# Optimization experiments

Measured on AMD Instinct MI355X. Metric: run time of the kernel, lower is better.

Reference implementation:

```python
import jax, jax.numpy as jnp
import numpy as np


def setup_inputs() -> dict:
    key = jax.random.key(0)
    k0, k1 = jax.random.split(key)
    B, S, T = 32, 512, 128
    return {
        "crf_score_0": jax.random.normal(k0, (B, S + 1, T, T), dtype=jnp.float32),
        "crf_score_1": jax.random.normal(k1, (B, S + 1, T), dtype=jnp.float32),
        "sof": 126,
        "eof": 127,
    }


def reference(crf_score_0, crf_score_1, sof, eof):
    # crf_score_0: [B, S+1, T, T], crf_score_1: [B, S+1, T]
    # Initial scores (note: original multiplies, not adds, at step 0)
    forscores = crf_score_0[:, 0, sof, :] * crf_score_1[:, 0, :]  # [B, T]

    # Move seq axis first for scan: [S, B, T, T] and [S, B, T]
    c0 = jnp.moveaxis(crf_score_0[:, 1:], 0, 1)
    c1 = jnp.moveaxis(crf_score_1[:, 1:], 0, 1)

    def fwd_step(fs, xs):
        t0, t1 = xs  # [B, T, T], [B, T]
        # cur[b, i, j] = fs[b, i] + t1[b, j] + t0[b, i, j]
        cur = fs[:, :, None] + t1[:, None, :] + t0
        new_fs = jnp.max(cur, axis=1)            # [B, T]
        bp = jnp.argmax(cur, axis=1).astype(jnp.int32)  # [B, T]
        return new_fs, bp

    _, back_points = jax.lax.scan(fwd_step, forscores, (c0, c1))  # bps: [S, B, T]

    # Backtrack exactly as the original loop: pointer starts at bp[-1][:, eof],
    # then for idx = S-1 .. 0: pointer = bp[idx][b, pointer]; decode[:, idx] = pointer.
    ptr0 = back_points[-1][:, eof]  # [B]

    def bwd_step(ptr, bp_t):
        new = jnp.take_along_axis(bp_t, ptr[:, None], axis=1)[:, 0]
        return new, new

    _, dec = jax.lax.scan(bwd_step, ptr0, back_points, reverse=True)  # [S, B]
    return dec.T.astype(jnp.int32)  # [B, S] decoded label indices
```

## Files before the change

### kernel.cpp

```cpp
#include <hip/hip_runtime.h>


constexpr int S   = 512;
constexpr int T   = 128;
constexpr int NSL = 8;
constexpr int CW  = 16;

using u64 = unsigned long long;
using u32 = unsigned int;

__device__ __forceinline__ void bar_lds() {
    asm volatile("s_waitcnt lgkmcnt(0)" ::: "memory");
    __builtin_amdgcn_s_barrier();
}
__device__ __forceinline__ u32 flipf(u32 u)   { return u ^ (0x80000000u | (u32)((int)u >> 31)); }
__device__ __forceinline__ u32 unflipf(u32 y) { return y ^ (0x80000000u | ~(u32)((int)y >> 31)); }
__device__ __forceinline__ u64 aload(const u64* p) {
    return __hip_atomic_load(p, __ATOMIC_RELAXED, __HIP_MEMORY_SCOPE_AGENT);
}
__device__ __forceinline__ void astore(u64* p, u64 v) {
    __hip_atomic_store(p, v, __ATOMIC_RELAXED, __HIP_MEMORY_SCOPE_AGENT);
}

#define GLDS(srcp, dstp) \
    __builtin_amdgcn_global_load_lds( \
        (const __attribute__((address_space(1))) void*)(srcp), \
        (__attribute__((address_space(3))) void*)(dstp), 16, 0, 0)

__global__ __launch_bounds__(256, 1)
void viterbi_fwdj(const float* __restrict__ c0, const float* __restrict__ c1,
                  const int* __restrict__ sofp,
                  u64* __restrict__ pub,
                  unsigned char* __restrict__ bp)
{
    __shared__ float fs_lds[T];
    __shared__ float t0s[2][T * CW];
    __shared__ u64   wpart[2][CW];

    const int g    = blockIdx.x;
    const int b    = g & 31;
    const int k    = g >> 5;
    const int tid  = (int)threadIdx.x;
    const int lane = tid & 63;

    const float* c0b = c0 + (size_t)b * (S + 1) * T * T;
    const float* c1b = c1 + (size_t)b * (S + 1) * T;
    u64* pubB = pub + (size_t)b * 2 * T;

    const bool is_cmp = tid >= 128;
    const int  ct  = tid - 128;
    const int  j   = ct & 15;
    const int  rb  = ct >> 4;
    const int  wv2 = (tid >> 6) - 2;

    auto STAGE = [&](int ss, int buf) {
        const float* srcbase = c0b + (size_t)ss * T * T + (size_t)k * CW;
        #pragma unroll
        for (int it = 0; it < 4; ++it) {
            const int q   = wv2 * 4 + it;
            const int row = q * 16 + (lane >> 2);
            const float* src = srcbase + (size_t)row * T + (lane & 3) * 4;
            float* dst = &t0s[buf][q * 256];
            GLDS(src, dst);
        }
    };

    if (tid < T) fs_lds[tid] = c0b[(size_t)sofp[0] * T + tid] * c1b[tid];
    float t1c = 0.f, t1n = 0.f;
    if (is_cmp) {
        STAGE(1, 1);
        t1c = c1b[(size_t)1 * T + k * CW + j];
    }
    asm volatile("s_waitcnt vmcnt(0)" ::: "memory");
    bar_lds();

    for (int s = 1; s <= S; ++s) {
        const int par = s & 1;

        if (is_cmp) {
            const float* tp = &t0s[par][0];
            const int r0 = rb * 16;
            u64 key;
            {
                float v = (fs_lds[r0] + t1c) + tp[r0 * CW + j];
                key = ((u64)flipf(__float_as_uint(v)) << 32) | (u32)(255 - r0);
            }
            #pragma unroll
            for (int r = 1; r < 16; ++r) {
                const int row = r0 + r;
                float v = (fs_lds[row] + t1c) + tp[row * CW + j];
                u64 kk = ((u64)flipf(__float_as_uint(v)) << 32) | (u32)(255 - row);
                if (kk > key) key = kk;
            }
            { u64 p = __shfl_xor(key, 16, 64); if (p > key) key = p; }
            { u64 p = __shfl_xor(key, 32, 64); if (p > key) key = p; }
            if ((ct & 63) < 16) wpart[wv2][j] = key;

            if (s < S) {
                STAGE(s + 1, par ^ 1);
                t1n = c1b[(size_t)(s + 1) * T + k * CW + j];
            }
        }
        bar_lds();

        if (is_cmp && ct < 16) {
            u64 kk = wpart[0][j];
            u64 k1 = wpart[1][j];
            if (k1 > kk) kk = k1;
            const u32 vb = unflipf((u32)(kk >> 32));
            const int ii = 255 - (int)(kk & 0xFFu);
            astore(&pubB[(size_t)par * T + k * CW + j], ((u64)vb << 32) | (u32)s);
            bp[((size_t)b * S + (s - 1)) * T + k * CW + j] = (unsigned char)ii;
            fs_lds[k * CW + j] = __uint_as_float(vb);
        }
        if (!is_cmp && (tid >> 4) != k) {
            const u64* p = &pubB[(size_t)par * T + tid];
            u64 v;
            do { v = aload(p); } while ((u32)v != (u32)s);
            fs_lds[tid] = __uint_as_float((u32)(v >> 32));
        }
        if (is_cmp) asm volatile("s_waitcnt vmcnt(0)" ::: "memory");
        bar_lds();

        t1c = t1n;
    }
}

__global__ __launch_bounds__(1024, 1)
void viterbi_bwd(const unsigned char* __restrict__ bp,
                 const int* __restrict__ eofp, int* __restrict__ out)
{
    __shared__ unsigned char lbp[S][T];
    const int b   = blockIdx.x;
    const int tid = (int)threadIdx.x;

    const uint4* s4 = (const uint4*)(bp + (size_t)b * S * T);
    uint4* d4 = (uint4*)&lbp[0][0];
    #pragma unroll
    for (int it = 0; it < 4; ++it) d4[tid + it * 1024] = s4[tid + it * 1024];
    __syncthreads();

    if (tid == 0) {
        int ptr = lbp[S - 1][eofp[0]];
        for (int idx = S - 1; idx >= 0; --idx) {
            ptr = lbp[idx][ptr];
            out[(size_t)b * S + idx] = ptr;
        }
    }
}

__global__ __launch_bounds__(1024, 1)
void viterbi_fused_fb(const float* __restrict__ c0, const float* __restrict__ c1,
                      const int* __restrict__ sofp, const int* __restrict__ eofp,
                      int* __restrict__ out)
{
    __shared__ float fs[2][T];
    __shared__ float pmax[32][T];
    __shared__ int   parg[32][T];
    __shared__ unsigned char bpl[S][T];

    const int b   = blockIdx.x;
    const int tid = (int)threadIdx.x;
    const int jq  = tid & 31;
    const int gg2 = tid >> 5;
    const int col = jq * 4;
    const int row = gg2 * 4;

    const float* c0b = c0 + (size_t)b * (S + 1) * T * T;
    const float* c1b = c1 + (size_t)b * (S + 1) * T;

    if (tid < T) {
        const int sof = sofp[0];
        fs[0][tid] = c0b[(size_t)sof * T + tid] * c1b[tid];
    }
    __syncthreads();

    const float* t0p = c0b + (size_t)T * T;
    float4 a0 = *(const float4*)(t0p + (size_t)(row + 0) * T + col);
    float4 a1 = *(const float4*)(t0p + (size_t)(row + 1) * T + col);
    float4 a2 = *(const float4*)(t0p + (size_t)(row + 2) * T + col);
    float4 a3 = *(const float4*)(t0p + (size_t)(row + 3) * T + col);
    float4 tv = *(const float4*)(c1b + T + col);

    int p = 0;
    for (int s = 1; s <= S; ++s) {
        float4 b0 = make_float4(0.f,0.f,0.f,0.f), b1 = b0, b2 = b0, b3 = b0, bt = b0;
        if (s < S) {
            const float* n0 = c0b + (size_t)(s + 1) * T * T;
            b0 = *(const float4*)(n0 + (size_t)(row + 0) * T + col);
            b1 = *(const float4*)(n0 + (size_t)(row + 1) * T + col);
            b2 = *(const float4*)(n0 + (size_t)(row + 2) * T + col);
            b3 = *(const float4*)(n0 + (size_t)(row + 3) * T + col);
            bt = *(const float4*)(c1b + (size_t)(s + 1) * T + col);
        }
        const float f0 = fs[p][row + 0];
        const float f1 = fs[p][row + 1];
        const float f2 = fs[p][row + 2];
        const float f3 = fs[p][row + 3];

        float bx, by, bz, bw; int ix, iy, iz, iw; float v;
        bx = (f0 + tv.x) + a0.x; ix = row;
        by = (f0 + tv.y) + a0.y; iy = row;
        bz = (f0 + tv.z) + a0.z; iz = row;
        bw = (f0 + tv.w) + a0.w; iw = row;
        v = (f1 + tv.x) + a1.x; if (v > bx) { bx = v; ix = row + 1; }
        v = (f1 + tv.y) + a1.y; if (v > by) { by = v; iy = row + 1; }
        v = (f1 + tv.z) + a1.z; if (v > bz) { bz = v; iz = row + 1; }
        v = (f1 + tv.w) + a1.w; if (v > bw) { bw = v; iw = row + 1; }
        v = (f2 + tv.x) + a2.x; if (v > bx) { bx = v; ix = row + 2; }
        v = (f2 + tv.y) + a2.y; if (v > by) { by = v; iy = row + 2; }
        v = (f2 + tv.z) + a2.z; if (v > bz) { bz = v; iz = row + 2; }
        v = (f2 + tv.w) + a2.w; if (v > bw) { bw = v; iw = row + 2; }
        v = (f3 + tv.x) + a3.x; if (v > bx) { bx = v; ix = row + 3; }
        v = (f3 + tv.y) + a3.y; if (v > by) { by = v; iy = row + 3; }
        v = (f3 + tv.z) + a3.z; if (v > bz) { bz = v; iz = row + 3; }
        v = (f3 + tv.w) + a3.w; if (v > bw) { bw = v; iw = row + 3; }

        *(float4*)&pmax[gg2][col] = make_float4(bx, by, bz, bw);
        *(int4*)  &parg[gg2][col] = make_int4(ix, iy, iz, iw);
        __syncthreads();

        if (tid < T) {
            float bb = pmax[0][tid];
            int   ii = parg[0][tid];
            #pragma unroll
            for (int qq2 = 1; qq2 < 32; ++qq2) {
                float vv = pmax[qq2][tid];
                if (vv > bb) { bb = vv; ii = parg[qq2][tid]; }
            }
            fs[p ^ 1][tid] = bb;
            bpl[s - 1][tid] = (unsigned char)ii;
        }
        __syncthreads();
        p ^= 1;
        a0 = b0; a1 = b1; a2 = b2; a3 = b3; tv = bt;
    }

    if (tid == 0) {
        const int eof = eofp[0];
        int ptr = bpl[S - 1][eof];
        for (int idx = S - 1; idx >= 0; --idx) {
            ptr = bpl[idx][ptr];
            out[(size_t)b * S + idx] = ptr;
        }
    }
}

extern "C" void kernel_launch(void* const* d_in, const int* in_sizes, int n_in,
                              void* d_out, int out_size, void* d_ws, size_t ws_size,
                              hipStream_t stream)
{
    const float* c0  = (const float*)d_in[0];
    const float* c1  = (const float*)d_in[1];
    const int*   sof = (const int*)d_in[2];
    const int*   eof = (const int*)d_in[3];
    int*         out = (int*)d_out;

    const int B = in_sizes[1] / ((S + 1) * T);

    const size_t pub_b = (size_t)B * 2 * T * 8;
    const size_t bp_b  = (size_t)B * S * T;
    if (B == 32 && ws_size >= pub_b + bp_b) {
        u64* pubw = (u64*)d_ws;
        unsigned char* bpw = (unsigned char*)d_ws + pub_b;
        viterbi_fwdj<<<dim3(B * NSL), dim3(256), 0, stream>>>(c0, c1, sof, pubw, bpw);
        viterbi_bwd<<<dim3(B), dim3(1024), 0, stream>>>(bpw, eof, out);
    } else {
        viterbi_fused_fb<<<dim3(B), dim3(1024), 0, stream>>>(c0, c1, sof, eof, out);
    }
}
```

Before: 846.9 us.

## Split forward Viterbi into dedicated poller and register-prefetching compute warps

The forward kernel is reorganised so the first 128 threads only poll remote slices' published scores into a double-buffered LDS array, while compute threads each own one column and 16 rows. Those compute threads hold two steps of transition data in registers instead of staging tiles through LDS with async global-to-LDS loads. The row reduction now uses in-register argmax plus three shuffles, which removes the wpart LDS reduction and one barrier per step. Publication switches to an atomic exchange. The trade-off is strided scalar global loads (16 per thread per step) and heavier register use, in exchange for a shorter per-step critical path.

```diff
diff --git a/kernel.cpp b/kernel.cpp
--- a/kernel.cpp
+++ b/kernel.cpp
@@ -4,7 +4,6 @@
 constexpr int S   = 512;
 constexpr int T   = 128;
 constexpr int NSL = 8;
-constexpr int CW  = 16;
 
 using u64 = unsigned long long;
 using u32 = unsigned int;
@@ -18,111 +17,112 @@
 __device__ __forceinline__ u64 aload(const u64* p) {
     return __hip_atomic_load(p, __ATOMIC_RELAXED, __HIP_MEMORY_SCOPE_AGENT);
 }
-__device__ __forceinline__ void astore(u64* p, u64 v) {
-    __hip_atomic_store(p, v, __ATOMIC_RELAXED, __HIP_MEMORY_SCOPE_AGENT);
-}
-
-#define GLDS(srcp, dstp) \
-    __builtin_amdgcn_global_load_lds( \
-        (const __attribute__((address_space(1))) void*)(srcp), \
-        (__attribute__((address_space(3))) void*)(dstp), 16, 0, 0)
+__device__ __forceinline__ void apub(u64* p, u64 v) {
+    (void)__hip_atomic_exchange(p, v, __ATOMIC_RELAXED, __HIP_MEMORY_SCOPE_AGENT);
+}
 
 __global__ __launch_bounds__(256, 1)
-void viterbi_fwdj(const float* __restrict__ c0, const float* __restrict__ c1,
+void viterbi_fwdx(const float* __restrict__ c0, const float* __restrict__ c1,
                   const int* __restrict__ sofp,
                   u64* __restrict__ pub,
                   unsigned char* __restrict__ bp)
 {
-    __shared__ float fs_lds[T];
-    __shared__ float t0s[2][T * CW];
-    __shared__ u64   wpart[2][CW];
-
-    const int g    = blockIdx.x;
-    const int b    = g & 31;
-    const int k    = g >> 5;
-    const int tid  = (int)threadIdx.x;
-    const int lane = tid & 63;
+    __shared__ float fs[2][T];
+
+    const int g   = blockIdx.x;
+    const int b   = g & 31;
+    const int k   = g >> 5;
+    const int tid = (int)threadIdx.x;
 
     const float* c0b = c0 + (size_t)b * (S + 1) * T * T;
     const float* c1b = c1 + (size_t)b * (S + 1) * T;
     u64* pubB = pub + (size_t)b * 2 * T;
 
-    const bool is_cmp = tid >= 128;
-    const int  ct  = tid - 128;
-    const int  j   = ct & 15;
-    const int  rb  = ct >> 4;
-    const int  wv2 = (tid >> 6) - 2;
-
-    auto STAGE = [&](int ss, int buf) {
-        const float* srcbase = c0b + (size_t)ss * T * T + (size_t)k * CW;
+    if (tid < 128) {
+        const int  col    = tid;
+        const bool remote = (col >> 4) != k;
+        fs[0][col] = c0b[(size_t)sofp[0] * T + col] * c1b[col];
+        bar_lds();
+        for (int s = 1; s <= S; ++s) {
+            if (remote) {
+                const u64* p = &pubB[(size_t)(s & 1) * T + col];
+                u64 v;
+                do { v = aload(p); } while ((u32)v != (u32)s);
+                fs[s & 1][col] = __uint_as_float((u32)(v >> 32));
+            }
+            bar_lds();
+        }
+    } else {
+        const int ct  = tid - 128;
+        const int jj  = ct >> 3;
+        const int ih  = ct & 7;
+        const int col = k * 16 + jj;
+        const int r0  = 16 * ih;
+        const u32 tieb = (u32)(255 - r0);
+
+        const float* pA = c0b + (size_t)1 * T * T + (size_t)r0 * T + col;
+        const float* pB = pA + T * T;
+        float a[16], c[16];
         #pragma unroll
-        for (int it = 0; it < 4; ++it) {
-            const int q   = wv2 * 4 + it;
-            const int row = q * 16 + (lane >> 2);
-            const float* src = srcbase + (size_t)row * T + (lane & 3) * 4;
-            float* dst = &t0s[buf][q * 256];
-            GLDS(src, dst);
-        }
-    };
-
-    if (tid < T) fs_lds[tid] = c0b[(size_t)sofp[0] * T + tid] * c1b[tid];
-    float t1c = 0.f, t1n = 0.f;
-    if (is_cmp) {
-        STAGE(1, 1);
-        t1c = c1b[(size_t)1 * T + k * CW + j];
-    }
-    asm volatile("s_waitcnt vmcnt(0)" ::: "memory");
-    bar_lds();
-
-    for (int s = 1; s <= S; ++s) {
-        const int par = s & 1;
-
-        if (is_cmp) {
-            const float* tp = &t0s[par][0];
-            const int r0 = rb * 16;
-            u64 key;
-            {
-                float v = (fs_lds[r0] + t1c) + tp[r0 * CW + j];
-                key = ((u64)flipf(__float_as_uint(v)) << 32) | (u32)(255 - r0);
-            }
-            #pragma unroll
-            for (int r = 1; r < 16; ++r) {
-                const int row = r0 + r;
-                float v = (fs_lds[row] + t1c) + tp[row * CW + j];
-                u64 kk = ((u64)flipf(__float_as_uint(v)) << 32) | (u32)(255 - row);
-                if (kk > key) key = kk;
-            }
-            { u64 p = __shfl_xor(key, 16, 64); if (p > key) key = p; }
-            { u64 p = __shfl_xor(key, 32, 64); if (p > key) key = p; }
-            if ((ct & 63) < 16) wpart[wv2][j] = key;
-
-            if (s < S) {
-                STAGE(s + 1, par ^ 1);
-                t1n = c1b[(size_t)(s + 1) * T + k * CW + j];
-            }
-        }
+        for (int i = 0; i < 16; ++i) a[i] = pA[i * T];
+        #pragma unroll
+        for (int i = 0; i < 16; ++i) c[i] = pB[i * T];
+        float tA = c1b[(size_t)1 * T + col];
+        float tB = c1b[(size_t)2 * T + col];
+        unsigned char* bpc = bp + (size_t)b * S * T + col;
         bar_lds();
 
-        if (is_cmp && ct < 16) {
-            u64 kk = wpart[0][j];
-            u64 k1 = wpart[1][j];
-            if (k1 > kk) kk = k1;
-            const u32 vb = unflipf((u32)(kk >> 32));
-            const int ii = 255 - (int)(kk & 0xFFu);
-            astore(&pubB[(size_t)par * T + k * CW + j], ((u64)vb << 32) | (u32)s);
-            bp[((size_t)b * S + (s - 1)) * T + k * CW + j] = (unsigned char)ii;
-            fs_lds[k * CW + j] = __uint_as_float(vb);
-        }
-        if (!is_cmp && (tid >> 4) != k) {
-            const u64* p = &pubB[(size_t)par * T + tid];
-            u64 v;
-            do { v = aload(p); } while ((u32)v != (u32)s);
-            fs_lds[tid] = __uint_as_float((u32)(v >> 32));
-        }
-        if (is_cmp) asm volatile("s_waitcnt vmcnt(0)" ::: "memory");
-        bar_lds();
-
-        t1c = t1n;
+        auto STEP = [&](int s, float (&arr)[16], const float*& pp, float& tc) {
+            const int par = s & 1;
+            const float* fsr = fs[par ^ 1];
+            float4 f0 = *(const float4*)&fsr[r0];
+            float4 f1 = *(const float4*)&fsr[r0 + 4];
+            float4 f2 = *(const float4*)&fsr[r0 + 8];
+            float4 f3 = *(const float4*)&fsr[r0 + 12];
+
+            float bv, v; int br;
+            bv = (f0.x + tc) + arr[0];  br = 0;
+            v = (f0.y + tc) + arr[1];  if (v > bv) { bv = v; br = 1; }
+            v = (f0.z + tc) + arr[2];  if (v > bv) { bv = v; br = 2; }
+            v = (f0.w + tc) + arr[3];  if (v > bv) { bv = v; br = 3; }
+            v = (f1.x + tc) + arr[4];  if (v > bv) { bv = v; br = 4; }
+            v = (f1.y + tc) + arr[5];  if (v > bv) { bv = v; br = 5; }
+            v = (f1.z + tc) + arr[6];  if (v > bv) { bv = v; br = 6; }
+            v = (f1.w + tc) + arr[7];  if (v > bv) { bv = v; br = 7; }
+            v = (f2.x + tc) + arr[8];  if (v > bv) { bv = v; br = 8; }
+            v = (f2.y + tc) + arr[9];  if (v > bv) { bv = v; br = 9; }
+            v = (f2.z + tc) + arr[10]; if (v > bv) { bv = v; br = 10; }
+            v = (f2.w + tc) + arr[11]; if (v > bv) { bv = v; br = 11; }
+            v = (f3.x + tc) + arr[12]; if (v > bv) { bv = v; br = 12; }
+            v = (f3.y + tc) + arr[13]; if (v > bv) { bv = v; br = 13; }
+            v = (f3.z + tc) + arr[14]; if (v > bv) { bv = v; br = 14; }
+            v = (f3.w + tc) + arr[15]; if (v > bv) { bv = v; br = 15; }
+
+            u64 key = ((u64)flipf(__float_as_uint(bv)) << 32) | (u32)(tieb - br);
+            { u64 p = __shfl_xor(key, 1, 64); if (p > key) key = p; }
+            { u64 p = __shfl_xor(key, 2, 64); if (p > key) key = p; }
+            { u64 p = __shfl_xor(key, 4, 64); if (p > key) key = p; }
+
+            if (ih == 0) {
+                const u32 vb = unflipf((u32)(key >> 32));
+                apub(&pubB[(size_t)par * T + col], ((u64)vb << 32) | (u32)s);
+                bpc[(size_t)(s - 1) * T] = (unsigned char)(255 - (int)(key & 0xFFu));
+                fs[par][col] = __uint_as_float(vb);
+            }
+
+            if (s + 2 <= S) {
+                pp += 2 * T * T;
+                #pragma unroll
+                for (int i = 0; i < 16; ++i) arr[i] = pp[i * T];
+                tc = c1b[(size_t)(s + 2) * T + col];
+            }
+            bar_lds();
+        };
+
+        for (int s = 1; s <= S; s += 2) {
+            STEP(s,     a, pA, tA);
+            STEP(s + 1, c, pB, tB);
+        }
     }
 }
 
@@ -154,7 +154,7 @@
                       const int* __restrict__ sofp, const int* __restrict__ eofp,
                       int* __restrict__ out)
 {
-    __shared__ float fs[2][T];
+    __shared__ float fsl[2][T];
     __shared__ float pmax[32][T];
     __shared__ int   parg[32][T];
     __shared__ unsigned char bpl[S][T];
@@ -171,7 +171,7 @@
 
     if (tid < T) {
         const int sof = sofp[0];
-        fs[0][tid] = c0b[(size_t)sof * T + tid] * c1b[tid];
+        fsl[0][tid] = c0b[(size_t)sof * T + tid] * c1b[tid];
     }
     __syncthreads();
 
@@ -193,10 +193,10 @@
             b3 = *(const float4*)(n0 + (size_t)(row + 3) * T + col);
             bt = *(const float4*)(c1b + (size_t)(s + 1) * T + col);
         }
-        const float f0 = fs[p][row + 0];
-        const float f1 = fs[p][row + 1];
-        const float f2 = fs[p][row + 2];
-        const float f3 = fs[p][row + 3];
+        const float f0 = fsl[p][row + 0];
+        const float f1 = fsl[p][row + 1];
+        const float f2 = fsl[p][row + 2];
+        const float f3 = fsl[p][row + 3];
 
         float bx, by, bz, bw; int ix, iy, iz, iw; float v;
         bx = (f0 + tv.x) + a0.x; ix = row;
@@ -228,7 +228,7 @@
                 float vv = pmax[qq2][tid];
                 if (vv > bb) { bb = vv; ii = parg[qq2][tid]; }
             }
-            fs[p ^ 1][tid] = bb;
+            fsl[p ^ 1][tid] = bb;
             bpl[s - 1][tid] = (unsigned char)ii;
         }
         __syncthreads();
@@ -263,7 +263,7 @@
     if (B == 32 && ws_size >= pub_b + bp_b) {
         u64* pubw = (u64*)d_ws;
         unsigned char* bpw = (unsigned char*)d_ws + pub_b;
-        viterbi_fwdj<<<dim3(B * NSL), dim3(256), 0, stream>>>(c0, c1, sof, pubw, bpw);
+        viterbi_fwdx<<<dim3(B * NSL), dim3(256), 0, stream>>>(c0, c1, sof, pubw, bpw);
         viterbi_bwd<<<dim3(B), dim3(1024), 0, stream>>>(bpw, eof, out);
     } else {
         viterbi_fused_fb<<<dim3(B), dim3(1024), 0, stream>>>(c0, c1, sof, eof, out);
```

After: 884.6 us. +4.5%, slower.
